# Optimization experiments

Hardware: AMD Instinct MI355X
Metric: run time of the kernel (lower is better)

## Reference

```python
import jax, jax.numpy as jnp
import numpy as np

NUM_USERS = 100000
NUM_RATINGS = 5
EMBED_DIM = 64
ATT_DIM = 16
B, G, L, S = 16384, 8, 50, 32


def setup_inputs() -> dict:
    key = jax.random.key(0)
    ks = jax.random.split(key, 16)
    inp = {
        # forward args (int / bool constants)
        "nodes": jax.random.randint(ks[0], (B, G), 0, NUM_USERS),
        "history_u": jax.random.randint(ks[1], (B, L), 0, NUM_USERS),
        "history_r": jax.random.randint(ks[2], (B, L), 0, NUM_RATINGS),
        "history_mask": jax.random.randint(ks[3], (B, L), 0, 2).astype(bool).at[:, 0].set(True),
        "social_adj": jax.random.randint(ks[4], (B, S), 0, NUM_USERS),
        "social_mask": jax.random.randint(ks[5], (B, S), 0, 2).astype(bool).at[:, 0].set(True),
        # learned parameters
        "features": jax.random.normal(ks[6], (NUM_USERS, EMBED_DIM), jnp.float32) * 0.02,
        "r_embed": jax.random.normal(ks[7], (NUM_RATINGS, EMBED_DIM), jnp.float32) * 0.02,
        "wg1": jax.random.normal(ks[8], (EMBED_DIM, ATT_DIM), jnp.float32) / np.sqrt(EMBED_DIM),
        "bg1": jnp.zeros((ATT_DIM,), jnp.float32),
        "wg2": jax.random.normal(ks[9], (ATT_DIM, 1), jnp.float32) / np.sqrt(ATT_DIM),
        "bg2": jnp.zeros((1,), jnp.float32),
        "w1": jax.random.normal(ks[10], (2 * EMBED_DIM, EMBED_DIM), jnp.float32) / np.sqrt(2 * EMBED_DIM),
        "b1": jnp.zeros((EMBED_DIM,), jnp.float32),
    }
    return inp


def _masked_mean(x, mask):
    # x: [B, N, D], mask: [B, N] float -> [B, D]
    denom = jnp.maximum(mask.sum(axis=1, keepdims=True), 1.0)
    return (x * mask[..., None]).sum(axis=1) / denom


def reference(nodes, history_u, history_r, history_mask, social_adj, social_mask,
              features, r_embed, wg1, bg1, wg2, bg2, w1, b1):
    dt = features.dtype
    # --- Group_Embedding: attention pooling over member embeddings ---
    members = features[nodes]                              # [B, G, D] gather
    h = jnp.tanh(members @ wg1 + bg1)                      # [B, G, 16]
    logits = (h @ wg2 + bg2)[..., 0]                       # [B, G]
    alpha = jax.nn.softmax(logits, axis=-1)
    self_feats = jnp.einsum('bg,bgd->bd', alpha, members)  # [B, D]

    # --- aggregator: ragged history (item+rating) + social neighbor means ---
    hm = history_mask.astype(dt)
    hist = features[history_u] + r_embed[history_r]        # [B, L, D] gather
    hist_mean = _masked_mean(hist, hm)                     # [B, D]

    sm = social_mask.astype(dt)
    soc_mean = _masked_mean(features[social_adj], sm)      # [B, D]

    neigh_feats = 0.5 * (hist_mean + soc_mean)             # [B, D]

    # --- concat -> linear -> relu ---
    combined = jnp.concatenate([self_feats, neigh_feats], axis=1)  # [B, 2D]
    return jax.nn.relu(combined @ w1 + b1)                 # [B, D]
```

## Files before the change

kernel.cpp:

```cpp
#include <hip/hip_runtime.h>
#include <cstdint>
#include <cstddef>

#define NUSERS 100000
#define BB 16384

static __device__ __forceinline__ unsigned short f2bf(float x) {
    unsigned u = __float_as_uint(x);
    u += 0x7FFF + ((u >> 16) & 1);
    return (unsigned short)(u >> 16);
}
static __device__ __forceinline__ float4 bf4_to_f4(ushort4 h) {
    float4 r;
    r.x = __uint_as_float((unsigned)h.x << 16);
    r.y = __uint_as_float((unsigned)h.y << 16);
    r.z = __uint_as_float((unsigned)h.z << 16);
    r.w = __uint_as_float((unsigned)h.w << 16);
    return r;
}

__global__ __launch_bounds__(256) void k0_scores(
    const float* __restrict__ features, const float* __restrict__ wg1,
    const float* __restrict__ bg1, const float* __restrict__ wg2,
    const float* __restrict__ bg2, float* __restrict__ Q,
    unsigned short* __restrict__ fbf)
{
    __shared__ float frow[16 * 68];
    __shared__ float wg1t[16 * 68];
    const int tid = threadIdx.x;
    const int blk = blockIdx.x;
    const float* fbase = features + (size_t)blk * 16 * 64;
    for (int i = tid; i < 1024; i += 256) {
        frow[(i >> 6) * 68 + (i & 63)] = fbase[i];
        wg1t[(i & 15) * 68 + (i >> 4)] = wg1[i];
    }
    __syncthreads();

    {
        const int base = tid * 4;
        const int row = base >> 6, col = base & 63;
        ushort4 o;
        o.x = f2bf(frow[row * 68 + col + 0]);
        o.y = f2bf(frow[row * 68 + col + 1]);
        o.z = f2bf(frow[row * 68 + col + 2]);
        o.w = f2bf(frow[row * 68 + col + 3]);
        *(ushort4*)(fbf + (size_t)blk * 1024 + base) = o;
    }

    const int k = tid & 15, ul = tid >> 4;
    float x = bg1[k];
    #pragma unroll
    for (int d4 = 0; d4 < 16; ++d4) {
        const float4 f = *(const float4*)&frow[ul * 68 + d4 * 4];
        const float4 w = *(const float4*)&wg1t[k * 68 + d4 * 4];
        x += f.x * w.x + f.y * w.y + f.z * w.z + f.w * w.w;
    }
    float xx = fminf(fmaxf(x, -9.f), 9.f);
    float e2 = __expf(2.f * xx);
    float th = (e2 - 1.f) / (e2 + 1.f);
    float t = th * wg2[k];
    t += __shfl_xor(t, 1);
    t += __shfl_xor(t, 2);
    t += __shfl_xor(t, 4);
    t += __shfl_xor(t, 8);
    if (k == 0) Q[blk * 16 + ul] = t + bg2[0];
}

__global__ __launch_bounds__(256) void k1_fuse(
    const int* __restrict__ nodes, const int* __restrict__ hist_u,
    const int* __restrict__ hist_r, const int* __restrict__ hist_m,
    const int* __restrict__ soc_a, const int* __restrict__ soc_m,
    const unsigned short* __restrict__ fbf, const float* __restrict__ r_embed,
    const float* __restrict__ Q, float* __restrict__ comb)
{
    __shared__ int   lcomp[4][96];
    __shared__ float wcomp[4][96];

    const int tid = threadIdx.x;
    const int lane = tid & 63;
    const int wv = tid >> 6;
    const int e = blockIdx.x * 4 + wv;
    const int sub = lane & 15;
    const int grp = lane >> 4;
    const char* fb = (const char*)fbf;

    lcomp[wv][lane] = 0;
    wcomp[wv][lane] = 0.f;
    if (lane < 32) { lcomp[wv][64 + lane] = 0; wcomp[wv][64 + lane] = 0.f; }

    const float4* re4p = (const float4*)r_embed;
    const float4 re0 = re4p[0 * 16 + sub];
    const float4 re1 = re4p[1 * 16 + sub];
    const float4 re2 = re4p[2 * 16 + sub];
    const float4 re3 = re4p[3 * 16 + sub];
    const float4 re4 = re4p[4 * 16 + sub];

    int nd = (lane < 8) ? nodes[e * 8 + lane] : 0;
    int hu = 0, hr = 0, hmv = 0;
    if (lane < 50) {
        hu  = hist_u[e * 50 + lane];
        hr  = hist_r[e * 50 + lane];
        hmv = hist_m[e * 50 + lane];
    }
    int sa = 0, sk = 0;
    if (lane < 32) {
        sa = soc_a[e * 32 + lane];
        sk = soc_m[e * 32 + lane];
    }

    uint64_t hb = __ballot(hmv != 0);
    const int hc = (int)__popcll(hb);
    int hrank = (int)__popcll(hb & ((1ull << lane) - 1));

    uint64_t sbm = __ballot(sk != 0);
    const int scn = (int)__popcll(sbm);
    int srank = (int)__popcll(sbm & ((1ull << lane) - 1));

    const float ih = 1.f / (float)hc;
    const float is = 1.f / (float)scn;
    const float hw = 0.5f * ih;
    const float sw = 0.5f * is;

    if (hmv) { lcomp[wv][hrank] = hu << 7; wcomp[wv][hrank] = hw; }
    if (sk)  { lcomp[wv][hc + srank] = sa << 7; wcomp[wv][hc + srank] = sw; }

    const int c0 = (int)__popcll(__ballot(hmv && hr == 0));
    const int c1 = (int)__popcll(__ballot(hmv && hr == 1));
    const int c2 = (int)__popcll(__ballot(hmv && hr == 2));
    const int c3 = (int)__popcll(__ballot(hmv && hr == 3));
    const int c4 = (int)__popcll(__ballot(hmv && hr == 4));

    float sc = (lane < 8) ? Q[nd] : -1e30f;
    float mx = sc;
    mx = fmaxf(mx, __shfl_xor(mx, 1));
    mx = fmaxf(mx, __shfl_xor(mx, 2));
    mx = fmaxf(mx, __shfl_xor(mx, 4));
    float ex = __expf(sc - mx);
    float sm = ex;
    sm += __shfl_xor(sm, 1);
    sm += __shfl_xor(sm, 2);
    sm += __shfl_xor(sm, 4);
    float al = ex / sm;

    int   pkA = lcomp[wv][lane];
    int   pkB = lcomp[wv][64 + (lane & 31)];
    float wgA = wcomp[wv][lane];
    float wgB = wcomp[wv][64 + (lane & 31)];
    const int n = hc + scn;

    float4 sf4;
    {
        float a0 = __shfl(al, grp);
        int   u0 = __shfl(nd, grp);
        float a1 = __shfl(al, 4 + grp);
        int   u1 = __shfl(nd, 4 + grp);
        const float4 v0 = bf4_to_f4(*(const ushort4*)(fb + ((unsigned)u0 << 7) + sub * 8));
        const float4 v1 = bf4_to_f4(*(const ushort4*)(fb + ((unsigned)u1 << 7) + sub * 8));
        sf4.x = a0 * v0.x + a1 * v1.x;
        sf4.y = a0 * v0.y + a1 * v1.y;
        sf4.z = a0 * v0.z + a1 * v1.z;
        sf4.w = a0 * v0.w + a1 * v1.w;
    }

    float4 nb4 = {0.f, 0.f, 0.f, 0.f};
    for (int base = 0; base < n; base += 16) {
        #pragma unroll
        for (int j = 0; j < 4; ++j) {
            const int cbase = base + j * 4;
            int off; float w;
            if (cbase < 64) {
                off = __shfl(pkA, cbase + grp);
                w   = __shfl(wgA, cbase + grp);
            } else {
                off = __shfl(pkB, cbase - 64 + grp);
                w   = __shfl(wgB, cbase - 64 + grp);
            }
            const float4 v = bf4_to_f4(*(const ushort4*)(fb + (unsigned)off + sub * 8));
            nb4.x += w * v.x; nb4.y += w * v.y;
            nb4.z += w * v.z; nb4.w += w * v.w;
        }
    }

#define XRED(v4)                                            \
    v4.x += __shfl_xor(v4.x, 16); v4.x += __shfl_xor(v4.x, 32); \
    v4.y += __shfl_xor(v4.y, 16); v4.y += __shfl_xor(v4.y, 32); \
    v4.z += __shfl_xor(v4.z, 16); v4.z += __shfl_xor(v4.z, 32); \
    v4.w += __shfl_xor(v4.w, 16); v4.w += __shfl_xor(v4.w, 32);
    XRED(sf4)
    XRED(nb4)
#undef XRED

    float f0 = hw * (float)c0, f1 = hw * (float)c1, f2 = hw * (float)c2,
          f3 = hw * (float)c3, f4 = hw * (float)c4;
    nb4.x += f0 * re0.x + f1 * re1.x + f2 * re2.x + f3 * re3.x + f4 * re4.x;
    nb4.y += f0 * re0.y + f1 * re1.y + f2 * re2.y + f3 * re3.y + f4 * re4.y;
    nb4.z += f0 * re0.z + f1 * re1.z + f2 * re2.z + f3 * re3.z + f4 * re4.z;
    nb4.w += f0 * re0.w + f1 * re1.w + f2 * re2.w + f3 * re3.w + f4 * re4.w;

    if (grp == 0) *(float4*)(comb + (size_t)e * 128 + sub * 4) = sf4;
    if (grp == 1) *(float4*)(comb + (size_t)e * 128 + 64 + sub * 4) = nb4;
}

__global__ __launch_bounds__(256) void k2_gemm(
    const float* __restrict__ comb, const float* __restrict__ w1,
    const float* __restrict__ b1, float* __restrict__ out)
{
    __shared__ float w1s[128 * 64];
    __shared__ float4 ct4[32 * 32];
    const int tid = threadIdx.x;
    const float4* w14 = (const float4*)w1;
    float4* w1s4 = (float4*)w1s;
    for (int i = tid; i < 2048; i += 256) w1s4[i] = w14[i];
    const float4* c4 = (const float4*)(comb + (size_t)blockIdx.x * 32 * 128);
    for (int i = tid; i < 1024; i += 256) ct4[i] = c4[i];
    __syncthreads();

    const int n = tid & 63, wv = tid >> 6;
    const float bv = b1[n];
    float acc[8] = {bv, bv, bv, bv, bv, bv, bv, bv};
    #pragma unroll
    for (int k4 = 0; k4 < 32; ++k4) {
        float w0  = w1s[(k4 * 4 + 0) * 64 + n];
        float w1v = w1s[(k4 * 4 + 1) * 64 + n];
        float w2v = w1s[(k4 * 4 + 2) * 64 + n];
        float w3v = w1s[(k4 * 4 + 3) * 64 + n];
        #pragma unroll
        for (int i = 0; i < 8; ++i) {
            float4 cv = ct4[(wv * 8 + i) * 32 + k4];
            acc[i] += cv.x * w0 + cv.y * w1v + cv.z * w2v + cv.w * w3v;
        }
    }
    const int row0 = blockIdx.x * 32 + wv * 8;
    #pragma unroll
    for (int i = 0; i < 8; ++i)
        out[(size_t)(row0 + i) * 64 + n] = fmaxf(acc[i], 0.f);
}

extern "C" void kernel_launch(void* const* d_in, const int* in_sizes, int n_in,
                              void* d_out, int out_size, void* d_ws, size_t ws_size,
                              hipStream_t stream)
{
    const int*   nodes    = (const int*)d_in[0];
    const int*   hu       = (const int*)d_in[1];
    const int*   hr       = (const int*)d_in[2];
    const int*   hm       = (const int*)d_in[3];
    const int*   sa       = (const int*)d_in[4];
    const int*   smk      = (const int*)d_in[5];
    const float* features = (const float*)d_in[6];
    const float* r_embed  = (const float*)d_in[7];
    const float* wg1      = (const float*)d_in[8];
    const float* bg1      = (const float*)d_in[9];
    const float* wg2      = (const float*)d_in[10];
    const float* bg2      = (const float*)d_in[11];
    const float* w1       = (const float*)d_in[12];
    const float* b1       = (const float*)d_in[13];
    float* out = (float*)d_out;

    float*          Q    = (float*)d_ws;
    unsigned short* fbf  = (unsigned short*)(Q + 131072);
    float*          comb = (float*)(fbf + (size_t)NUSERS * 64);

    k0_scores<<<NUSERS / 16, 256, 0, stream>>>(features, wg1, bg1, wg2, bg2, Q, fbf);
    k1_fuse<<<BB / 4, 256, 0, stream>>>(nodes, hu, hr, hm, sa, smk,
                                        fbf, r_embed, Q, comb);
    k2_gemm<<<BB / 32, 256, 0, stream>>>(comb, w1, b1, out);
}
```

Before: 139.2 us.

## Fuse final linear+ReLU into gather kernel and vectorize feature staging in k0

Removes the separate GEMM kernel: each wave writes its 128-wide combined vector to shared memory and computes the 64 output columns directly, reading w1 from global/L2. This eliminates the comb round-trip through global memory and one kernel launch. k0 now loads features with one float4 per thread and converts to bf16 straight from registers instead of re-reading LDS. The fused GEMM reads w1 per wave without reuse across rows, relying on cache hits.

```diff
diff --git a/kernel.cpp b/kernel.cpp
--- a/kernel.cpp
+++ b/kernel.cpp
@@ -29,31 +29,34 @@
     __shared__ float wg1t[16 * 68];
     const int tid = threadIdx.x;
     const int blk = blockIdx.x;
-    const float* fbase = features + (size_t)blk * 16 * 64;
-    for (int i = tid; i < 1024; i += 256) {
-        frow[(i >> 6) * 68 + (i & 63)] = fbase[i];
-        wg1t[(i & 15) * 68 + (i >> 4)] = wg1[i];
+
+    const float4 v = ((const float4*)(features + (size_t)blk * 1024))[tid];
+    {
+        const int row = tid >> 4, q = tid & 15;
+        *(float4*)&frow[row * 68 + q * 4] = v;
+    }
+    {
+        const float4 w = ((const float4*)wg1)[tid];
+        const int d = tid >> 2, k0 = (tid & 3) * 4;
+        wg1t[(k0 + 0) * 68 + d] = w.x;
+        wg1t[(k0 + 1) * 68 + d] = w.y;
+        wg1t[(k0 + 2) * 68 + d] = w.z;
+        wg1t[(k0 + 3) * 68 + d] = w.w;
+    }
+    {
+        ushort4 o;
+        o.x = f2bf(v.x); o.y = f2bf(v.y); o.z = f2bf(v.z); o.w = f2bf(v.w);
+        *(ushort4*)(fbf + (size_t)blk * 1024 + tid * 4) = o;
     }
     __syncthreads();
-
-    {
-        const int base = tid * 4;
-        const int row = base >> 6, col = base & 63;
-        ushort4 o;
-        o.x = f2bf(frow[row * 68 + col + 0]);
-        o.y = f2bf(frow[row * 68 + col + 1]);
-        o.z = f2bf(frow[row * 68 + col + 2]);
-        o.w = f2bf(frow[row * 68 + col + 3]);
-        *(ushort4*)(fbf + (size_t)blk * 1024 + base) = o;
-    }
 
     const int k = tid & 15, ul = tid >> 4;
     float x = bg1[k];
     #pragma unroll
     for (int d4 = 0; d4 < 16; ++d4) {
-        const float4 f = *(const float4*)&frow[ul * 68 + d4 * 4];
-        const float4 w = *(const float4*)&wg1t[k * 68 + d4 * 4];
-        x += f.x * w.x + f.y * w.y + f.z * w.z + f.w * w.w;
+        const float4 f  = *(const float4*)&frow[ul * 68 + d4 * 4];
+        const float4 wv = *(const float4*)&wg1t[k * 68 + d4 * 4];
+        x += f.x * wv.x + f.y * wv.y + f.z * wv.z + f.w * wv.w;
     }
     float xx = fminf(fmaxf(x, -9.f), 9.f);
     float e2 = __expf(2.f * xx);
@@ -71,10 +74,12 @@
     const int* __restrict__ hist_r, const int* __restrict__ hist_m,
     const int* __restrict__ soc_a, const int* __restrict__ soc_m,
     const unsigned short* __restrict__ fbf, const float* __restrict__ r_embed,
-    const float* __restrict__ Q, float* __restrict__ comb)
+    const float* __restrict__ Q, const float* __restrict__ w1,
+    const float* __restrict__ b1, float* __restrict__ out)
 {
     __shared__ int   lcomp[4][96];
     __shared__ float wcomp[4][96];
+    __shared__ float combs[4][128];
 
     const int tid = threadIdx.x;
     const int lane = tid & 63;
@@ -197,43 +202,20 @@
     nb4.z += f0 * re0.z + f1 * re1.z + f2 * re2.z + f3 * re3.z + f4 * re4.z;
     nb4.w += f0 * re0.w + f1 * re1.w + f2 * re2.w + f3 * re3.w + f4 * re4.w;
 
-    if (grp == 0) *(float4*)(comb + (size_t)e * 128 + sub * 4) = sf4;
-    if (grp == 1) *(float4*)(comb + (size_t)e * 128 + 64 + sub * 4) = nb4;
-}
-
-__global__ __launch_bounds__(256) void k2_gemm(
-    const float* __restrict__ comb, const float* __restrict__ w1,
-    const float* __restrict__ b1, float* __restrict__ out)
-{
-    __shared__ float w1s[128 * 64];
-    __shared__ float4 ct4[32 * 32];
-    const int tid = threadIdx.x;
-    const float4* w14 = (const float4*)w1;
-    float4* w1s4 = (float4*)w1s;
-    for (int i = tid; i < 2048; i += 256) w1s4[i] = w14[i];
-    const float4* c4 = (const float4*)(comb + (size_t)blockIdx.x * 32 * 128);
-    for (int i = tid; i < 1024; i += 256) ct4[i] = c4[i];
-    __syncthreads();
-
-    const int n = tid & 63, wv = tid >> 6;
-    const float bv = b1[n];
-    float acc[8] = {bv, bv, bv, bv, bv, bv, bv, bv};
-    #pragma unroll
+    if (grp == 0) *(float4*)&combs[wv][sub * 4] = sf4;
+    if (grp == 1) *(float4*)&combs[wv][64 + sub * 4] = nb4;
+
+    const int col = lane;
+    float y = b1[col];
+    #pragma unroll 8
     for (int k4 = 0; k4 < 32; ++k4) {
-        float w0  = w1s[(k4 * 4 + 0) * 64 + n];
-        float w1v = w1s[(k4 * 4 + 1) * 64 + n];
-        float w2v = w1s[(k4 * 4 + 2) * 64 + n];
-        float w3v = w1s[(k4 * 4 + 3) * 64 + n];
-        #pragma unroll
-        for (int i = 0; i < 8; ++i) {
-            float4 cv = ct4[(wv * 8 + i) * 32 + k4];
-            acc[i] += cv.x * w0 + cv.y * w1v + cv.z * w2v + cv.w * w3v;
-        }
-    }
-    const int row0 = blockIdx.x * 32 + wv * 8;
-    #pragma unroll
-    for (int i = 0; i < 8; ++i)
-        out[(size_t)(row0 + i) * 64 + n] = fmaxf(acc[i], 0.f);
+        const float4 c = *(const float4*)&combs[wv][k4 * 4];
+        y += c.x * w1[(k4 * 4 + 0) * 64 + col]
+           + c.y * w1[(k4 * 4 + 1) * 64 + col]
+           + c.z * w1[(k4 * 4 + 2) * 64 + col]
+           + c.w * w1[(k4 * 4 + 3) * 64 + col];
+    }
+    out[(size_t)e * 64 + col] = fmaxf(y, 0.f);
 }
 
 extern "C" void kernel_launch(void* const* d_in, const int* in_sizes, int n_in,
@@ -258,10 +240,8 @@
 
     float*          Q    = (float*)d_ws;
     unsigned short* fbf  = (unsigned short*)(Q + 131072);
-    float*          comb = (float*)(fbf + (size_t)NUSERS * 64);
 
     k0_scores<<<NUSERS / 16, 256, 0, stream>>>(features, wg1, bg1, wg2, bg2, Q, fbf);
     k1_fuse<<<BB / 4, 256, 0, stream>>>(nodes, hu, hr, hm, sa, smk,
-                                        fbf, r_embed, Q, comb);
-    k2_gemm<<<BB / 32, 256, 0, stream>>>(comb, w1, b1, out);
-}
+                                        fbf, r_embed, Q, w1, b1, out);
+}
```

After: 139.7 us. No clear change (+0.4%).
